# Kernel tuning notes

Measured on AMD Instinct MI355X. Metric: run time of the kernel, lower is better.

The kernel has to match this reference:

```python
import jax, jax.numpy as jnp
import numpy as np

N_NODES = 100000
N_EDGES = 1000000
N_GRAPHS = 128
BN_EPS = 1e-5


def setup_inputs() -> dict:
    key = jax.random.key(0)
    ks = jax.random.split(key, 20)
    H = 64
    F = 128
    C = 10
    inp = {
        'x': jax.random.normal(ks[0], (N_NODES, F), jnp.float32),
        'edge_index': jax.random.randint(ks[1], (2, N_EDGES), 0, N_NODES, jnp.int64),
        'batch': jax.random.randint(ks[2], (N_NODES,), 0, N_GRAPHS, jnp.int64),
        'W1_0': jax.random.normal(ks[3], (F, H), jnp.float32) * 0.05,
        'bn_g_0': jax.random.uniform(ks[4], (H,), jnp.float32) + 0.5,
        'bn_b_0': jax.random.normal(ks[5], (H,), jnp.float32) * 0.1,
        'bn_m_0': jax.random.normal(ks[6], (H,), jnp.float32) * 0.1,
        'bn_v_0': jax.random.uniform(ks[7], (H,), jnp.float32) + 0.5,
        'W2_0': jax.random.normal(ks[8], (H, H), jnp.float32) * 0.1,
        'W1_r': jax.random.normal(ks[9], (3, H, H), jnp.float32) * 0.1,
        'bn_g_r': jax.random.uniform(ks[10], (3, H), jnp.float32) + 0.5,
        'bn_b_r': jax.random.normal(ks[11], (3, H), jnp.float32) * 0.1,
        'bn_m_r': jax.random.normal(ks[12], (3, H), jnp.float32) * 0.1,
        'bn_v_r': jax.random.uniform(ks[13], (3, H), jnp.float32) + 0.5,
        'W2_r': jax.random.normal(ks[14], (3, H, H), jnp.float32) * 0.1,
        'lin1_W': jax.random.normal(ks[15], (H, H), jnp.float32) * 0.1,
        'lin2_W': jax.random.normal(ks[16], (H, C), jnp.float32) * 0.1,
        'lin2_b': jax.random.normal(ks[17], (C,), jnp.float32) * 0.1,
    }
    return inp


def _gin_conv(x, src, dst, W1, g, b, m, v, W2):
    # sum aggregation of neighbor messages (PyG GINConv, eps=0)
    agg = jax.ops.segment_sum(x[src], dst, num_segments=N_NODES)
    h = (x + agg) @ W1                           # [N, H], Linear no bias
    h = (h - m) * jax.lax.rsqrt(v + BN_EPS) * g + b  # BatchNorm1d (eval)
    h = jax.nn.relu(h)
    h = jax.nn.relu(h @ W2)
    return h


def reference(x, edge_index, batch, W1_0, bn_g_0, bn_b_0, bn_m_0, bn_v_0, W2_0,
              W1_r, bn_g_r, bn_b_r, bn_m_r, bn_v_r, W2_r, lin1_W, lin2_W, lin2_b):
    src, dst = edge_index[0], edge_index[1]
    h = _gin_conv(x, src, dst, W1_0, bn_g_0, bn_b_0, bn_m_0, bn_v_0, W2_0)
    for i in range(W1_r.shape[0]):
        h = _gin_conv(h, src, dst, W1_r[i], bn_g_r[i], bn_b_r[i], bn_m_r[i], bn_v_r[i], W2_r[i])
    # global mean pool over graphs
    sums = jax.ops.segment_sum(h, batch, num_segments=N_GRAPHS)
    cnts = jax.ops.segment_sum(jnp.ones((h.shape[0], 1), h.dtype), batch, num_segments=N_GRAPHS)
    pooled = sums / jnp.maximum(cnts, 1.0)
    z = jax.nn.relu(pooled @ lin1_W)  # dropout inactive (eval)
    z = z @ lin2_W + lin2_b
    return jax.nn.log_softmax(z, axis=-1)
```

## Files before the change

### kernel.cpp

```cpp
#include <hip/hip_runtime.h>
#include <hip/hip_bf16.h>
#include <hip/hip_fp16.h>

#define HDIM 64
#define NGRAPH 128
#define NCLS 10
#define BN_EPS 1e-5f
#define SCAN_CHUNK 1024


__global__ void count_kernel(const int* __restrict__ dst, int* __restrict__ deg, int E) {
    int e = blockIdx.x * blockDim.x + threadIdx.x;
    if (e < E) atomicAdd(&deg[dst[e]], 1);
}

__global__ void scan1_kernel(const int* __restrict__ deg, int* __restrict__ part, int N) {
    __shared__ int sh[256];
    int base = blockIdx.x * SCAN_CHUNK + threadIdx.x * 4;
    int s = 0;
#pragma unroll
    for (int i = 0; i < 4; i++) { int idx = base + i; if (idx < N) s += deg[idx]; }
    sh[threadIdx.x] = s; __syncthreads();
    for (int off = 128; off > 0; off >>= 1) {
        if (threadIdx.x < off) sh[threadIdx.x] += sh[threadIdx.x + off];
        __syncthreads();
    }
    if (threadIdx.x == 0) part[blockIdx.x] = sh[0];
}

__global__ void scan2_kernel(int* __restrict__ part, int nblk, int* __restrict__ row_ptr, int N, int E) {
    __shared__ int sh[256];
    int v = (threadIdx.x < nblk) ? part[threadIdx.x] : 0;
    sh[threadIdx.x] = v; __syncthreads();
    for (int off = 1; off < 256; off <<= 1) {
        int t = (threadIdx.x >= off) ? sh[threadIdx.x - off] : 0;
        __syncthreads();
        sh[threadIdx.x] += t;
        __syncthreads();
    }
    if (threadIdx.x < nblk) part[threadIdx.x] = sh[threadIdx.x] - v;
    if (threadIdx.x == 0) row_ptr[N] = E;
}

__global__ void scan3_kernel(const int* __restrict__ deg, const int* __restrict__ part,
                             int* __restrict__ row_ptr, int* __restrict__ cursor, int N) {
    __shared__ int sh[256];
    int tbase = blockIdx.x * SCAN_CHUNK + threadIdx.x * 4;
    int vals[4]; int s = 0;
#pragma unroll
    for (int i = 0; i < 4; i++) { int idx = tbase + i; vals[i] = (idx < N) ? deg[idx] : 0; s += vals[i]; }
    sh[threadIdx.x] = s; __syncthreads();
    for (int off = 1; off < 256; off <<= 1) {
        int t = (threadIdx.x >= off) ? sh[threadIdx.x - off] : 0;
        __syncthreads();
        sh[threadIdx.x] += t;
        __syncthreads();
    }
    int run = part[blockIdx.x] + sh[threadIdx.x] - s;
#pragma unroll
    for (int i = 0; i < 4; i++) {
        int idx = tbase + i;
        if (idx < N) { row_ptr[idx] = run; cursor[idx] = run; run += vals[i]; }
    }
}


__global__ void __launch_bounds__(256) fused_scatter_gemm0_kernel(
        const int* __restrict__ src, const int* __restrict__ dst,
        int* __restrict__ cursor, int* __restrict__ col, int E, int eb,
        const float* __restrict__ X, const float* __restrict__ W,
        __half* __restrict__ Y, int N) {
    __shared__ float Xs[64 * 64];
    __shared__ float Ws[64 * 64];

    if ((int)blockIdx.x < eb) {
        int e = blockIdx.x * 256 + threadIdx.x;
        if (e < E) {
            int pos = atomicAdd(&cursor[dst[e]], 1);
            col[pos] = src[e];
        }
        return;
    }

    const int tid = threadIdx.x;
    const int base = (blockIdx.x - eb) * 64;
    const int ti = tid >> 4;
    const int tj = tid & 15;
    float4 acc[4];
#pragma unroll
    for (int a = 0; a < 4; a++) acc[a] = make_float4(0.f, 0.f, 0.f, 0.f);

    for (int kh = 0; kh < 2; kh++) {
        {
            const float4* Wv = reinterpret_cast<const float4*>(W + kh * 64 * 64);
            float4* Wsv = reinterpret_cast<float4*>(Ws);
            for (int i = tid; i < 1024; i += 256) Wsv[i] = Wv[i];
        }
        for (int i = tid; i < 1024; i += 256) {
            int r = i & 63;
            int c4 = i >> 6;
            int n = base + r;
            float4 v = make_float4(0.f, 0.f, 0.f, 0.f);
            if (n < N) v = *reinterpret_cast<const float4*>(X + (size_t)n * 128 + kh * 64 + c4 * 4);
            Xs[(c4 * 4 + 0) * 64 + r] = v.x;
            Xs[(c4 * 4 + 1) * 64 + r] = v.y;
            Xs[(c4 * 4 + 2) * 64 + r] = v.z;
            Xs[(c4 * 4 + 3) * 64 + r] = v.w;
        }
        __syncthreads();

#pragma unroll 4
        for (int k = 0; k < 64; k++) {
            float4 xv = *reinterpret_cast<const float4*>(&Xs[k * 64 + 4 * ti]);
            float4 wv = *reinterpret_cast<const float4*>(&Ws[k * 64 + 4 * tj]);
            acc[0].x += xv.x * wv.x; acc[0].y += xv.x * wv.y; acc[0].z += xv.x * wv.z; acc[0].w += xv.x * wv.w;
            acc[1].x += xv.y * wv.x; acc[1].y += xv.y * wv.y; acc[1].z += xv.y * wv.z; acc[1].w += xv.y * wv.w;
            acc[2].x += xv.z * wv.x; acc[2].y += xv.z * wv.y; acc[2].z += xv.z * wv.z; acc[2].w += xv.z * wv.w;
            acc[3].x += xv.w * wv.x; acc[3].y += xv.w * wv.y; acc[3].z += xv.w * wv.z; acc[3].w += xv.w * wv.w;
        }
        __syncthreads();
    }

#pragma unroll
    for (int a = 0; a < 4; a++) {
        int n = base + 4 * ti + a;
        if (n < N) {
            __half2* yp = reinterpret_cast<__half2*>(Y + (size_t)n * 64 + 4 * tj);
            yp[0] = __floats2half2_rn(acc[a].x, acc[a].y);
            yp[1] = __floats2half2_rn(acc[a].z, acc[a].w);
        }
    }
}


template<bool RELU>
__global__ void __launch_bounds__(256) gemm_tiled_kernel(const float* __restrict__ X,
                                                         const float* __restrict__ W,
                                                         float* __restrict__ Y, int N) {
    __shared__ float Xs[64 * 64];
    __shared__ float Ws[64 * 64];
    const int tid = threadIdx.x;
    const int base = blockIdx.x * 64;

    {
        const float4* Wv = reinterpret_cast<const float4*>(W);
        float4* Wsv = reinterpret_cast<float4*>(Ws);
        for (int i = tid; i < 1024; i += 256) Wsv[i] = Wv[i];
    }
    for (int i = tid; i < 1024; i += 256) {
        int r = i & 63;
        int c4 = i >> 6;
        int n = base + r;
        float4 v = make_float4(0.f, 0.f, 0.f, 0.f);
        if (n < N) v = *reinterpret_cast<const float4*>(X + (size_t)n * 64 + c4 * 4);
        Xs[(c4 * 4 + 0) * 64 + r] = v.x;
        Xs[(c4 * 4 + 1) * 64 + r] = v.y;
        Xs[(c4 * 4 + 2) * 64 + r] = v.z;
        Xs[(c4 * 4 + 3) * 64 + r] = v.w;
    }
    __syncthreads();

    const int ti = tid >> 4;
    const int tj = tid & 15;
    float4 acc[4];
#pragma unroll
    for (int a = 0; a < 4; a++) acc[a] = make_float4(0.f, 0.f, 0.f, 0.f);

#pragma unroll 4
    for (int k = 0; k < 64; k++) {
        float4 xv = *reinterpret_cast<const float4*>(&Xs[k * 64 + 4 * ti]);
        float4 wv = *reinterpret_cast<const float4*>(&Ws[k * 64 + 4 * tj]);
        acc[0].x += xv.x * wv.x; acc[0].y += xv.x * wv.y; acc[0].z += xv.x * wv.z; acc[0].w += xv.x * wv.w;
        acc[1].x += xv.y * wv.x; acc[1].y += xv.y * wv.y; acc[1].z += xv.y * wv.z; acc[1].w += xv.y * wv.w;
        acc[2].x += xv.z * wv.x; acc[2].y += xv.z * wv.y; acc[2].z += xv.z * wv.z; acc[2].w += xv.z * wv.w;
        acc[3].x += xv.w * wv.x; acc[3].y += xv.w * wv.y; acc[3].z += xv.w * wv.z; acc[3].w += xv.w * wv.w;
    }

#pragma unroll
    for (int a = 0; a < 4; a++) {
        int n = base + 4 * ti + a;
        if (n < N) {
            float4 o = acc[a];
            if (RELU) {
                o.x = fmaxf(o.x, 0.f); o.y = fmaxf(o.y, 0.f);
                o.z = fmaxf(o.z, 0.f); o.w = fmaxf(o.w, 0.f);
            }
            *reinterpret_cast<float4*>(Y + (size_t)n * 64 + 4 * tj) = o;
        }
    }
}


__global__ void __launch_bounds__(256) gemm_pair_kernel(const float* __restrict__ H,
                                                        const float* __restrict__ W2,
                                                        const float* __restrict__ W1n,
                                                        __half* __restrict__ Y, int N) {
    __shared__ float Hs[64 * 64];
    __shared__ float W2s[64 * 64];
    __shared__ float W1s[64 * 64];
    const int tid = threadIdx.x;
    const int base = blockIdx.x * 64;

    {
        const float4* a = reinterpret_cast<const float4*>(W2);
        const float4* c = reinterpret_cast<const float4*>(W1n);
        float4* b = reinterpret_cast<float4*>(W2s);
        float4* d = reinterpret_cast<float4*>(W1s);
        for (int i = tid; i < 1024; i += 256) { b[i] = a[i]; d[i] = c[i]; }
    }
    for (int i = tid; i < 1024; i += 256) {
        int r = i & 63;
        int c4 = i >> 6;
        int n = base + r;
        float4 v = make_float4(0.f, 0.f, 0.f, 0.f);
        if (n < N) v = *reinterpret_cast<const float4*>(H + (size_t)n * 64 + c4 * 4);
        Hs[(c4 * 4 + 0) * 64 + r] = v.x;
        Hs[(c4 * 4 + 1) * 64 + r] = v.y;
        Hs[(c4 * 4 + 2) * 64 + r] = v.z;
        Hs[(c4 * 4 + 3) * 64 + r] = v.w;
    }
    __syncthreads();

    const int ti = tid >> 4;
    const int tj = tid & 15;
    float4 acc[4];
#pragma unroll
    for (int a = 0; a < 4; a++) acc[a] = make_float4(0.f, 0.f, 0.f, 0.f);

#pragma unroll 4
    for (int k = 0; k < 64; k++) {
        float4 xv = *reinterpret_cast<const float4*>(&Hs[k * 64 + 4 * ti]);
        float4 wv = *reinterpret_cast<const float4*>(&W2s[k * 64 + 4 * tj]);
        acc[0].x += xv.x * wv.x; acc[0].y += xv.x * wv.y; acc[0].z += xv.x * wv.z; acc[0].w += xv.x * wv.w;
        acc[1].x += xv.y * wv.x; acc[1].y += xv.y * wv.y; acc[1].z += xv.y * wv.z; acc[1].w += xv.y * wv.w;
        acc[2].x += xv.z * wv.x; acc[2].y += xv.z * wv.y; acc[2].z += xv.z * wv.z; acc[2].w += xv.z * wv.w;
        acc[3].x += xv.w * wv.x; acc[3].y += xv.w * wv.y; acc[3].z += xv.w * wv.z; acc[3].w += xv.w * wv.w;
    }
    __syncthreads();

#pragma unroll
    for (int a = 0; a < 4; a++) {
        float4 o = acc[a];
        o.x = fmaxf(o.x, 0.f); o.y = fmaxf(o.y, 0.f);
        o.z = fmaxf(o.z, 0.f); o.w = fmaxf(o.w, 0.f);
        *reinterpret_cast<float4*>(&Hs[(4 * ti + a) * 64 + 4 * tj]) = o;
    }
    __syncthreads();

    float4 acc2[4];
#pragma unroll
    for (int a = 0; a < 4; a++) acc2[a] = make_float4(0.f, 0.f, 0.f, 0.f);

#pragma unroll 4
    for (int k = 0; k < 64; k++) {
        float z0 = Hs[(4 * ti + 0) * 64 + k];
        float z1 = Hs[(4 * ti + 1) * 64 + k];
        float z2 = Hs[(4 * ti + 2) * 64 + k];
        float z3 = Hs[(4 * ti + 3) * 64 + k];
        float4 wv = *reinterpret_cast<const float4*>(&W1s[k * 64 + 4 * tj]);
        acc2[0].x += z0 * wv.x; acc2[0].y += z0 * wv.y; acc2[0].z += z0 * wv.z; acc2[0].w += z0 * wv.w;
        acc2[1].x += z1 * wv.x; acc2[1].y += z1 * wv.y; acc2[1].z += z1 * wv.z; acc2[1].w += z1 * wv.w;
        acc2[2].x += z2 * wv.x; acc2[2].y += z2 * wv.y; acc2[2].z += z2 * wv.z; acc2[2].w += z2 * wv.w;
        acc2[3].x += z3 * wv.x; acc2[3].y += z3 * wv.y; acc2[3].z += z3 * wv.z; acc2[3].w += z3 * wv.w;
    }

#pragma unroll
    for (int a = 0; a < 4; a++) {
        int n = base + 4 * ti + a;
        if (n < N) {
            __half2* yp = reinterpret_cast<__half2*>(Y + (size_t)n * 64 + 4 * tj);
            yp[0] = __floats2half2_rn(acc2[a].x, acc2[a].y);
            yp[1] = __floats2half2_rn(acc2[a].z, acc2[a].w);
        }
    }
}


__global__ void agg_bn_relu_kernel(const __half* __restrict__ y, const int* __restrict__ rp,
                                   const int* __restrict__ col,
                                   const float* __restrict__ gam, const float* __restrict__ bet,
                                   const float* __restrict__ mu, const float* __restrict__ var,
                                   float* __restrict__ out, int N) {
    int wid = (blockIdx.x * blockDim.x + threadIdx.x) >> 6;
    int lane = threadIdx.x & 63;
    if (wid >= N) return;
    int grp = lane >> 5;
    int fl  = lane & 31;
    int beg = rp[wid], end = rp[wid + 1];

    float2 acc = make_float2(0.f, 0.f);
    if (grp == 0) {
        float2 f = __half22float2(*reinterpret_cast<const __half2*>(y + (size_t)wid * 64 + fl * 2));
        acc.x += f.x; acc.y += f.y;
    }
    int e = beg + grp;
    for (; e + 6 < end; e += 8) {
        int s0 = col[e], s1 = col[e + 2], s2 = col[e + 4], s3 = col[e + 6];
        float2 a0 = __half22float2(*reinterpret_cast<const __half2*>(y + (size_t)s0 * 64 + fl * 2));
        float2 a1 = __half22float2(*reinterpret_cast<const __half2*>(y + (size_t)s1 * 64 + fl * 2));
        float2 a2 = __half22float2(*reinterpret_cast<const __half2*>(y + (size_t)s2 * 64 + fl * 2));
        float2 a3 = __half22float2(*reinterpret_cast<const __half2*>(y + (size_t)s3 * 64 + fl * 2));
        acc.x += a0.x + a1.x + a2.x + a3.x;
        acc.y += a0.y + a1.y + a2.y + a3.y;
    }
    for (; e < end; e += 2) {
        float2 a = __half22float2(*reinterpret_cast<const __half2*>(y + (size_t)col[e] * 64 + fl * 2));
        acc.x += a.x; acc.y += a.y;
    }

    acc.x += __shfl_down(acc.x, 32);
    acc.y += __shfl_down(acc.y, 32);

    if (grp == 0) {
        int f0 = fl * 2, f1 = f0 + 1;
        float sc0 = gam[f0] * rsqrtf(var[f0] + BN_EPS);
        float sc1 = gam[f1] * rsqrtf(var[f1] + BN_EPS);
        float2 o;
        o.x = fmaxf(acc.x * sc0 + (bet[f0] - mu[f0] * sc0), 0.f);
        o.y = fmaxf(acc.y * sc1 + (bet[f1] - mu[f1] * sc1), 0.f);
        *reinterpret_cast<float2*>(out + (size_t)wid * 64 + f0) = o;
    }
}


__global__ void __launch_bounds__(256) pool_partial_kernel(const float* __restrict__ h,
                                                           const int* __restrict__ batch,
                                                           float* __restrict__ partial,
                                                           int* __restrict__ pcnt, int N) {
    __shared__ float ls[NGRAPH * 64];
    __shared__ int lc[NGRAPH];
    for (int i = threadIdx.x; i < NGRAPH * 64; i += 256) ls[i] = 0.f;
    if (threadIdx.x < NGRAPH) lc[threadIdx.x] = 0;
    __syncthreads();
    int lane = threadIdx.x & 63;
    int gwave = blockIdx.x * 4 + (threadIdx.x >> 6);
    int nwaves = gridDim.x * 4;
#pragma unroll 4
    for (int n = gwave; n < N; n += nwaves) {
        int g = batch[n];
        atomicAdd(&ls[g * 64 + lane], h[(size_t)n * 64 + lane]);
        if (lane == 0) atomicAdd(&lc[g], 1);
    }
    __syncthreads();
    for (int i = threadIdx.x; i < NGRAPH * 64; i += 256)
        partial[(size_t)blockIdx.x * NGRAPH * 64 + i] = ls[i];
    if (threadIdx.x < NGRAPH) pcnt[blockIdx.x * NGRAPH + threadIdx.x] = lc[threadIdx.x];
}


__global__ void head_kernel(const float* __restrict__ partial, const int* __restrict__ pcnt, int P,
                            const float* __restrict__ lin1, const float* __restrict__ lin2,
                            const float* __restrict__ b2, float* __restrict__ out) {
    int g = blockIdx.x;
    int j = threadIdx.x;
    __shared__ float p[64];
    __shared__ float z1[64];
    __shared__ float z2[NCLS];
    __shared__ int csh[64];
    float s = 0.f;
    for (int b = 0; b < P; b++) s += partial[(size_t)b * NGRAPH * 64 + g * 64 + j];
    int c = 0;
    for (int b = j; b < P; b += 64) c += pcnt[b * NGRAPH + g];
    csh[j] = c; __syncthreads();
    if (j == 0) { int t = 0; for (int k = 0; k < 64; k++) t += csh[k]; csh[0] = t; }
    __syncthreads();
    float cnt = fmaxf((float)csh[0], 1.f);
    p[j] = s / cnt;
    __syncthreads();
    float a = 0.f;
#pragma unroll
    for (int k = 0; k < 64; k++) a += p[k] * lin1[k * 64 + j];
    z1[j] = fmaxf(a, 0.f);
    __syncthreads();
    if (j < NCLS) {
        float t = b2[j];
#pragma unroll
        for (int k = 0; k < 64; k++) t += z1[k] * lin2[k * NCLS + j];
        z2[j] = t;
    }
    __syncthreads();
    if (j < NCLS) {
        float mx = -1e30f;
#pragma unroll
        for (int c2 = 0; c2 < NCLS; c2++) mx = fmaxf(mx, z2[c2]);
        float se = 0.f;
#pragma unroll
        for (int c2 = 0; c2 < NCLS; c2++) se += expf(z2[c2] - mx);
        out[g * NCLS + j] = z2[j] - mx - logf(se);
    }
}


extern "C" void kernel_launch(void* const* d_in, const int* in_sizes, int n_in,
                              void* d_out, int out_size, void* d_ws, size_t ws_size,
                              hipStream_t stream) {
    const float* x     = (const float*)d_in[0];
    const int*   ei    = (const int*)d_in[1];
    const int*   batch = (const int*)d_in[2];
    const float* W1_0  = (const float*)d_in[3];
    const float* g0    = (const float*)d_in[4];
    const float* b0    = (const float*)d_in[5];
    const float* m0    = (const float*)d_in[6];
    const float* v0    = (const float*)d_in[7];
    const float* W2_0  = (const float*)d_in[8];
    const float* W1r   = (const float*)d_in[9];
    const float* gr    = (const float*)d_in[10];
    const float* br    = (const float*)d_in[11];
    const float* mr    = (const float*)d_in[12];
    const float* vr    = (const float*)d_in[13];
    const float* W2r   = (const float*)d_in[14];
    const float* lin1  = (const float*)d_in[15];
    const float* lin2  = (const float*)d_in[16];
    const float* b2    = (const float*)d_in[17];

    const int N = in_sizes[0] / 128;
    const int E = in_sizes[1] / 2;
    const int* src = ei;
    const int* dst = ei + E;

    char* p = (char*)d_ws;
    auto alloc = [&](size_t bytes) -> char* {
        char* r = p;
        p += (bytes + 255) & ~(size_t)255;
        return r;
    };
    int*    deg     = (int*)alloc((size_t)N * 4);
    int*    row_ptr = (int*)alloc((size_t)(N + 1) * 4);
    int*    cursor  = (int*)alloc((size_t)N * 4);
    int*    col     = (int*)alloc((size_t)E * 4);
    int*    part    = (int*)alloc(256 * 4);
    float*  hA      = (float*)alloc((size_t)N * 64 * 4);
    __half* y16     = (__half*)alloc((size_t)N * 64 * 2);
    size_t used = (size_t)(p - (char*)d_ws);
    size_t per_block = ((size_t)NGRAPH * 64 * 4) + ((size_t)NGRAPH * 4) + 512;
    size_t remain = (ws_size > used) ? (ws_size - used) : 0;
    int P = (int)(remain / per_block);
    if (P > 256) P = 256;
    if (P < 1) P = 1;
    float* partial = (float*)alloc((size_t)P * NGRAPH * 64 * 4);
    int*   pcnt    = (int*)alloc((size_t)P * NGRAPH * 4);
    (void)n_in; (void)out_size;

    hipMemsetAsync(deg, 0, (size_t)N * 4, stream);

    int eb = (E + 255) / 256;
    count_kernel<<<eb, 256, 0, stream>>>(dst, deg, E);
    int nblk = (N + SCAN_CHUNK - 1) / SCAN_CHUNK;
    scan1_kernel<<<nblk, 256, 0, stream>>>(deg, part, N);
    scan2_kernel<<<1, 256, 0, stream>>>(part, nblk, row_ptr, N, E);
    scan3_kernel<<<nblk, 256, 0, stream>>>(deg, part, row_ptr, cursor, N);

    int mb = (N + 63) / 64;
    int ab = (N * 64 + 255) / 256;

    fused_scatter_gemm0_kernel<<<eb + mb, 256, 0, stream>>>(src, dst, cursor, col, E, eb,
                                                            x, W1_0, y16, N);
    agg_bn_relu_kernel<<<ab, 256, 0, stream>>>(y16, row_ptr, col, g0, b0, m0, v0, hA, N);

    gemm_pair_kernel<<<mb, 256, 0, stream>>>(hA, W2_0, W1r, y16, N);
    agg_bn_relu_kernel<<<ab, 256, 0, stream>>>(y16, row_ptr, col, gr, br, mr, vr, hA, N);

    gemm_pair_kernel<<<mb, 256, 0, stream>>>(hA, W2r, W1r + 4096, y16, N);
    agg_bn_relu_kernel<<<ab, 256, 0, stream>>>(y16, row_ptr, col, gr + 64, br + 64, mr + 64, vr + 64, hA, N);

    gemm_pair_kernel<<<mb, 256, 0, stream>>>(hA, W2r + 4096, W1r + 8192, y16, N);
    agg_bn_relu_kernel<<<ab, 256, 0, stream>>>(y16, row_ptr, col, gr + 128, br + 128, mr + 128, vr + 128, hA, N);

    gemm_tiled_kernel<true><<<mb, 256, 0, stream>>>(hA, W2r + 8192, hA, N);

    pool_partial_kernel<<<P, 256, 0, stream>>>(hA, batch, partial, pcnt, N);
    head_kernel<<<NGRAPH, 64, 0, stream>>>(partial, pcnt, P, lin1, lin2, b2, (float*)d_out);
}
```

Measured before the change: 644.7 us.

## Use fp16 MFMA for the 64x64 dense layers with pre-transposed weights

Replaces the FP32 register-tiled SIMT GEMMs (the pair kernel and the last layer) with MFMA 16x16x32 fp16 matrix instructions. A small prep kernel converts and transposes the seven 64x64 weight matrices to fp16 once per call. Activations are cast to fp16 in padded shared memory and accumulated in fp32. The aim is to cut the ALU and LDS cost of the GEMM phases, at the cost of fp16 rounding on inputs and intermediates and one extra launch.

```diff
diff --git a/kernel.cpp b/kernel.cpp
--- a/kernel.cpp
+++ b/kernel.cpp
@@ -7,6 +7,11 @@
 #define NCLS 10
 #define BN_EPS 1e-5f
 #define SCAN_CHUNK 1024
+#define LDH 72
+
+typedef _Float16 h16;
+typedef __attribute__((ext_vector_type(8))) _Float16 f16x8;
+typedef __attribute__((ext_vector_type(4))) float f32x4;
 
 
 __global__ void count_kernel(const int* __restrict__ dst, int* __restrict__ deg, int E) {
@@ -61,6 +66,21 @@
     for (int i = 0; i < 4; i++) {
         int idx = tbase + i;
         if (idx < N) { row_ptr[idx] = run; cursor[idx] = run; run += vals[i]; }
+    }
+}
+
+
+__global__ void prep_weights_kernel(const float* __restrict__ W2_0,
+                                    const float* __restrict__ W2r,
+                                    const float* __restrict__ W1r,
+                                    h16* __restrict__ wt) {
+    int b = blockIdx.x;
+    const float* src = (b == 0) ? W2_0 : (b <= 3) ? W2r + (size_t)(b - 1) * 4096
+                                                  : W1r + (size_t)(b - 4) * 4096;
+    h16* dst = wt + (size_t)b * 4096;
+    for (int i = threadIdx.x; i < 4096; i += 256) {
+        int k = i >> 6, j = i & 63;
+        dst[j * 64 + k] = (h16)src[k * 64 + j];
     }
 }
 
@@ -133,145 +153,148 @@
 }
 
 
-template<bool RELU>
-__global__ void __launch_bounds__(256) gemm_tiled_kernel(const float* __restrict__ X,
-                                                         const float* __restrict__ W,
-                                                         float* __restrict__ Y, int N) {
-    __shared__ float Xs[64 * 64];
-    __shared__ float Ws[64 * 64];
+__global__ void __launch_bounds__(256) gemm_pair_mfma(const float* __restrict__ H,
+                                                      const h16* __restrict__ Wt2,
+                                                      const h16* __restrict__ Wt1,
+                                                      __half* __restrict__ Y, int N) {
+    __shared__ h16 Xs[64 * LDH];
+    __shared__ h16 W2s[64 * LDH];
+    __shared__ h16 W1s[64 * LDH];
     const int tid = threadIdx.x;
     const int base = blockIdx.x * 64;
 
-    {
-        const float4* Wv = reinterpret_cast<const float4*>(W);
-        float4* Wsv = reinterpret_cast<float4*>(Ws);
-        for (int i = tid; i < 1024; i += 256) Wsv[i] = Wv[i];
-    }
-    for (int i = tid; i < 1024; i += 256) {
-        int r = i & 63;
-        int c4 = i >> 6;
-        int n = base + r;
+#pragma unroll
+    for (int it = 0; it < 4; ++it) {
+        int idx = it * 256 + tid;
+        int row = idx >> 4, q = idx & 15;
         float4 v = make_float4(0.f, 0.f, 0.f, 0.f);
-        if (n < N) v = *reinterpret_cast<const float4*>(X + (size_t)n * 64 + c4 * 4);
-        Xs[(c4 * 4 + 0) * 64 + r] = v.x;
-        Xs[(c4 * 4 + 1) * 64 + r] = v.y;
-        Xs[(c4 * 4 + 2) * 64 + r] = v.z;
-        Xs[(c4 * 4 + 3) * 64 + r] = v.w;
-    }
-    __syncthreads();
-
-    const int ti = tid >> 4;
-    const int tj = tid & 15;
-    float4 acc[4];
-#pragma unroll
-    for (int a = 0; a < 4; a++) acc[a] = make_float4(0.f, 0.f, 0.f, 0.f);
-
-#pragma unroll 4
-    for (int k = 0; k < 64; k++) {
-        float4 xv = *reinterpret_cast<const float4*>(&Xs[k * 64 + 4 * ti]);
-        float4 wv = *reinterpret_cast<const float4*>(&Ws[k * 64 + 4 * tj]);
-        acc[0].x += xv.x * wv.x; acc[0].y += xv.x * wv.y; acc[0].z += xv.x * wv.z; acc[0].w += xv.x * wv.w;
-        acc[1].x += xv.y * wv.x; acc[1].y += xv.y * wv.y; acc[1].z += xv.y * wv.z; acc[1].w += xv.y * wv.w;
-        acc[2].x += xv.z * wv.x; acc[2].y += xv.z * wv.y; acc[2].z += xv.z * wv.z; acc[2].w += xv.z * wv.w;
-        acc[3].x += xv.w * wv.x; acc[3].y += xv.w * wv.y; acc[3].z += xv.w * wv.z; acc[3].w += xv.w * wv.w;
-    }
-
-#pragma unroll
-    for (int a = 0; a < 4; a++) {
-        int n = base + 4 * ti + a;
-        if (n < N) {
-            float4 o = acc[a];
-            if (RELU) {
-                o.x = fmaxf(o.x, 0.f); o.y = fmaxf(o.y, 0.f);
-                o.z = fmaxf(o.z, 0.f); o.w = fmaxf(o.w, 0.f);
-            }
-            *reinterpret_cast<float4*>(Y + (size_t)n * 64 + 4 * tj) = o;
-        }
-    }
-}
-
-
-__global__ void __launch_bounds__(256) gemm_pair_kernel(const float* __restrict__ H,
-                                                        const float* __restrict__ W2,
-                                                        const float* __restrict__ W1n,
-                                                        __half* __restrict__ Y, int N) {
-    __shared__ float Hs[64 * 64];
-    __shared__ float W2s[64 * 64];
-    __shared__ float W1s[64 * 64];
+        int n = base + row;
+        if (n < N) v = *reinterpret_cast<const float4*>(H + (size_t)n * 64 + q * 4);
+        h16* d = &Xs[row * LDH + q * 4];
+        d[0] = (h16)v.x; d[1] = (h16)v.y; d[2] = (h16)v.z; d[3] = (h16)v.w;
+    }
+#pragma unroll
+    for (int it = 0; it < 2; ++it) {
+        int idx = it * 256 + tid;
+        int row = idx >> 3, q = idx & 7;
+        *reinterpret_cast<f16x8*>(&W2s[row * LDH + q * 8]) =
+            *reinterpret_cast<const f16x8*>(Wt2 + row * 64 + q * 8);
+        *reinterpret_cast<f16x8*>(&W1s[row * LDH + q * 8]) =
+            *reinterpret_cast<const f16x8*>(Wt1 + row * 64 + q * 8);
+    }
+    __syncthreads();
+
+    const int w  = tid >> 6;
+    const int l  = tid & 63;
+    const int lr = l & 15;
+    const int lk = l >> 4;
+
+    f16x8 a0 = *reinterpret_cast<const f16x8*>(&Xs[(16 * w + lr) * LDH + lk * 8]);
+    f16x8 a1 = *reinterpret_cast<const f16x8*>(&Xs[(16 * w + lr) * LDH + 32 + lk * 8]);
+    f32x4 acc[4];
+#pragma unroll
+    for (int t = 0; t < 4; ++t) {
+        f16x8 b0 = *reinterpret_cast<const f16x8*>(&W2s[(16 * t + lr) * LDH + lk * 8]);
+        f16x8 b1 = *reinterpret_cast<const f16x8*>(&W2s[(16 * t + lr) * LDH + 32 + lk * 8]);
+        f32x4 c = {0.f, 0.f, 0.f, 0.f};
+        c = __builtin_amdgcn_mfma_f32_16x16x32_f16(a0, b0, c, 0, 0, 0);
+        c = __builtin_amdgcn_mfma_f32_16x16x32_f16(a1, b1, c, 0, 0, 0);
+        acc[t] = c;
+    }
+#pragma unroll
+    for (int t = 0; t < 4; ++t)
+#pragma unroll
+        for (int r = 0; r < 4; ++r)
+            Xs[(16 * w + lk * 4 + r) * LDH + 16 * t + lr] = (h16)fmaxf(acc[t][r], 0.f);
+    __syncthreads();
+
+    f16x8 z0 = *reinterpret_cast<const f16x8*>(&Xs[(16 * w + lr) * LDH + lk * 8]);
+    f16x8 z1 = *reinterpret_cast<const f16x8*>(&Xs[(16 * w + lr) * LDH + 32 + lk * 8]);
+    f32x4 acc2[4];
+#pragma unroll
+    for (int t = 0; t < 4; ++t) {
+        f16x8 b0 = *reinterpret_cast<const f16x8*>(&W1s[(16 * t + lr) * LDH + lk * 8]);
+        f16x8 b1 = *reinterpret_cast<const f16x8*>(&W1s[(16 * t + lr) * LDH + 32 + lk * 8]);
+        f32x4 c = {0.f, 0.f, 0.f, 0.f};
+        c = __builtin_amdgcn_mfma_f32_16x16x32_f16(z0, b0, c, 0, 0, 0);
+        c = __builtin_amdgcn_mfma_f32_16x16x32_f16(z1, b1, c, 0, 0, 0);
+        acc2[t] = c;
+    }
+#pragma unroll
+    for (int t = 0; t < 4; ++t)
+#pragma unroll
+        for (int r = 0; r < 4; ++r)
+            W2s[(16 * w + lk * 4 + r) * LDH + 16 * t + lr] = (h16)acc2[t][r];
+    __syncthreads();
+
+#pragma unroll
+    for (int it = 0; it < 2; ++it) {
+        int idx = it * 256 + tid;
+        int row = idx >> 3, q = idx & 7;
+        int n = base + row;
+        if (n < N)
+            *reinterpret_cast<f16x8*>(reinterpret_cast<h16*>(Y) + (size_t)n * 64 + q * 8) =
+                *reinterpret_cast<const f16x8*>(&W2s[row * LDH + q * 8]);
+    }
+}
+
+
+__global__ void __launch_bounds__(256) gemm_last_mfma(const float* __restrict__ H,
+                                                      const h16* __restrict__ Wt,
+                                                      float* __restrict__ Y, int N) {
+    __shared__ h16 Xs[64 * LDH];
+    __shared__ h16 Ws[64 * LDH];
+    __shared__ float Zf[64 * 68];
     const int tid = threadIdx.x;
     const int base = blockIdx.x * 64;
 
-    {
-        const float4* a = reinterpret_cast<const float4*>(W2);
-        const float4* c = reinterpret_cast<const float4*>(W1n);
-        float4* b = reinterpret_cast<float4*>(W2s);
-        float4* d = reinterpret_cast<float4*>(W1s);
-        for (int i = tid; i < 1024; i += 256) { b[i] = a[i]; d[i] = c[i]; }
-    }
-    for (int i = tid; i < 1024; i += 256) {
-        int r = i & 63;
-        int c4 = i >> 6;
-        int n = base + r;
+#pragma unroll
+    for (int it = 0; it < 4; ++it) {
+        int idx = it * 256 + tid;
+        int row = idx >> 4, q = idx & 15;
         float4 v = make_float4(0.f, 0.f, 0.f, 0.f);
-        if (n < N) v = *reinterpret_cast<const float4*>(H + (size_t)n * 64 + c4 * 4);
-        Hs[(c4 * 4 + 0) * 64 + r] = v.x;
-        Hs[(c4 * 4 + 1) * 64 + r] = v.y;
-        Hs[(c4 * 4 + 2) * 64 + r] = v.z;
-        Hs[(c4 * 4 + 3) * 64 + r] = v.w;
-    }
-    __syncthreads();
-
-    const int ti = tid >> 4;
-    const int tj = tid & 15;
-    float4 acc[4];
-#pragma unroll
-    for (int a = 0; a < 4; a++) acc[a] = make_float4(0.f, 0.f, 0.f, 0.f);
-
-#pragma unroll 4
-    for (int k = 0; k < 64; k++) {
-        float4 xv = *reinterpret_cast<const float4*>(&Hs[k * 64 + 4 * ti]);
-        float4 wv = *reinterpret_cast<const float4*>(&W2s[k * 64 + 4 * tj]);
-        acc[0].x += xv.x * wv.x; acc[0].y += xv.x * wv.y; acc[0].z += xv.x * wv.z; acc[0].w += xv.x * wv.w;
-        acc[1].x += xv.y * wv.x; acc[1].y += xv.y * wv.y; acc[1].z += xv.y * wv.z; acc[1].w += xv.y * wv.w;
-        acc[2].x += xv.z * wv.x; acc[2].y += xv.z * wv.y; acc[2].z += xv.z * wv.z; acc[2].w += xv.z * wv.w;
-        acc[3].x += xv.w * wv.x; acc[3].y += xv.w * wv.y; acc[3].z += xv.w * wv.z; acc[3].w += xv.w * wv.w;
-    }
-    __syncthreads();
-
-#pragma unroll
-    for (int a = 0; a < 4; a++) {
-        float4 o = acc[a];
-        o.x = fmaxf(o.x, 0.f); o.y = fmaxf(o.y, 0.f);
-        o.z = fmaxf(o.z, 0.f); o.w = fmaxf(o.w, 0.f);
-        *reinterpret_cast<float4*>(&Hs[(4 * ti + a) * 64 + 4 * tj]) = o;
-    }
-    __syncthreads();
-
-    float4 acc2[4];
-#pragma unroll
-    for (int a = 0; a < 4; a++) acc2[a] = make_float4(0.f, 0.f, 0.f, 0.f);
-
-#pragma unroll 4
-    for (int k = 0; k < 64; k++) {
-        float z0 = Hs[(4 * ti + 0) * 64 + k];
-        float z1 = Hs[(4 * ti + 1) * 64 + k];
-        float z2 = Hs[(4 * ti + 2) * 64 + k];
-        float z3 = Hs[(4 * ti + 3) * 64 + k];
-        float4 wv = *reinterpret_cast<const float4*>(&W1s[k * 64 + 4 * tj]);
-        acc2[0].x += z0 * wv.x; acc2[0].y += z0 * wv.y; acc2[0].z += z0 * wv.z; acc2[0].w += z0 * wv.w;
-        acc2[1].x += z1 * wv.x; acc2[1].y += z1 * wv.y; acc2[1].z += z1 * wv.z; acc2[1].w += z1 * wv.w;
-        acc2[2].x += z2 * wv.x; acc2[2].y += z2 * wv.y; acc2[2].z += z2 * wv.z; acc2[2].w += z2 * wv.w;
-        acc2[3].x += z3 * wv.x; acc2[3].y += z3 * wv.y; acc2[3].z += z3 * wv.z; acc2[3].w += z3 * wv.w;
-    }
-
-#pragma unroll
-    for (int a = 0; a < 4; a++) {
-        int n = base + 4 * ti + a;
-        if (n < N) {
-            __half2* yp = reinterpret_cast<__half2*>(Y + (size_t)n * 64 + 4 * tj);
-            yp[0] = __floats2half2_rn(acc2[a].x, acc2[a].y);
-            yp[1] = __floats2half2_rn(acc2[a].z, acc2[a].w);
-        }
+        int n = base + row;
+        if (n < N) v = *reinterpret_cast<const float4*>(H + (size_t)n * 64 + q * 4);
+        h16* d = &Xs[row * LDH + q * 4];
+        d[0] = (h16)v.x; d[1] = (h16)v.y; d[2] = (h16)v.z; d[3] = (h16)v.w;
+    }
+#pragma unroll
+    for (int it = 0; it < 2; ++it) {
+        int idx = it * 256 + tid;
+        int row = idx >> 3, q = idx & 7;
+        *reinterpret_cast<f16x8*>(&Ws[row * LDH + q * 8]) =
+            *reinterpret_cast<const f16x8*>(Wt + row * 64 + q * 8);
+    }
+    __syncthreads();
+
+    const int w  = tid >> 6;
+    const int l  = tid & 63;
+    const int lr = l & 15;
+    const int lk = l >> 4;
+
+    f16x8 a0 = *reinterpret_cast<const f16x8*>(&Xs[(16 * w + lr) * LDH + lk * 8]);
+    f16x8 a1 = *reinterpret_cast<const f16x8*>(&Xs[(16 * w + lr) * LDH + 32 + lk * 8]);
+#pragma unroll
+    for (int t = 0; t < 4; ++t) {
+        f16x8 b0 = *reinterpret_cast<const f16x8*>(&Ws[(16 * t + lr) * LDH + lk * 8]);
+        f16x8 b1 = *reinterpret_cast<const f16x8*>(&Ws[(16 * t + lr) * LDH + 32 + lk * 8]);
+        f32x4 c = {0.f, 0.f, 0.f, 0.f};
+        c = __builtin_amdgcn_mfma_f32_16x16x32_f16(a0, b0, c, 0, 0, 0);
+        c = __builtin_amdgcn_mfma_f32_16x16x32_f16(a1, b1, c, 0, 0, 0);
+#pragma unroll
+        for (int r = 0; r < 4; ++r)
+            Zf[(16 * w + lk * 4 + r) * 68 + 16 * t + lr] = fmaxf(c[r], 0.f);
+    }
+    __syncthreads();
+
+#pragma unroll
+    for (int it = 0; it < 4; ++it) {
+        int idx = it * 256 + tid;
+        int row = idx >> 4, q = idx & 15;
+        int n = base + row;
+        if (n < N)
+            *reinterpret_cast<float4*>(Y + (size_t)n * 64 + q * 4) =
+                *reinterpret_cast<const float4*>(&Zf[row * 68 + q * 4]);
     }
 }
 
@@ -431,6 +454,7 @@
     int*    part    = (int*)alloc(256 * 4);
     float*  hA      = (float*)alloc((size_t)N * 64 * 4);
     __half* y16     = (__half*)alloc((size_t)N * 64 * 2);
+    h16*    wt      = (h16*)alloc((size_t)7 * 4096 * 2);
     size_t used = (size_t)(p - (char*)d_ws);
     size_t per_block = ((size_t)NGRAPH * 64 * 4) + ((size_t)NGRAPH * 4) + 512;
     size_t remain = (ws_size > used) ? (ws_size - used) : 0;
@@ -443,6 +467,7 @@
 
     hipMemsetAsync(deg, 0, (size_t)N * 4, stream);
 
+    prep_weights_kernel<<<7, 256, 0, stream>>>(W2_0, W2r, W1r, wt);
     int eb = (E + 255) / 256;
     count_kernel<<<eb, 256, 0, stream>>>(dst, deg, E);
     int nblk = (N + SCAN_CHUNK - 1) / SCAN_CHUNK;
@@ -457,16 +482,16 @@
                                                             x, W1_0, y16, N);
     agg_bn_relu_kernel<<<ab, 256, 0, stream>>>(y16, row_ptr, col, g0, b0, m0, v0, hA, N);
 
-    gemm_pair_kernel<<<mb, 256, 0, stream>>>(hA, W2_0, W1r, y16, N);
+    gemm_pair_mfma<<<mb, 256, 0, stream>>>(hA, wt + 0 * 4096, wt + 4 * 4096, y16, N);
     agg_bn_relu_kernel<<<ab, 256, 0, stream>>>(y16, row_ptr, col, gr, br, mr, vr, hA, N);
 
-    gemm_pair_kernel<<<mb, 256, 0, stream>>>(hA, W2r, W1r + 4096, y16, N);
+    gemm_pair_mfma<<<mb, 256, 0, stream>>>(hA, wt + 1 * 4096, wt + 5 * 4096, y16, N);
     agg_bn_relu_kernel<<<ab, 256, 0, stream>>>(y16, row_ptr, col, gr + 64, br + 64, mr + 64, vr + 64, hA, N);
 
-    gemm_pair_kernel<<<mb, 256, 0, stream>>>(hA, W2r + 4096, W1r + 8192, y16, N);
+    gemm_pair_mfma<<<mb, 256, 0, stream>>>(hA, wt + 2 * 4096, wt + 6 * 4096, y16, N);
     agg_bn_relu_kernel<<<ab, 256, 0, stream>>>(y16, row_ptr, col, gr + 128, br + 128, mr + 128, vr + 128, hA, N);
 
-    gemm_tiled_kernel<true><<<mb, 256, 0, stream>>>(hA, W2r + 8192, hA, N);
+    gemm_last_mfma<<<mb, 256, 0, stream>>>(hA, wt + 3 * 4096, hA, N);
 
     pool_partial_kernel<<<P, 256, 0, stream>>>(hA, batch, partial, pcnt, N);
     head_kernel<<<NGRAPH, 64, 0, stream>>>(partial, pcnt, P, lin1, lin2, b2, (float*)d_out);
```

New measurement: 593.2 us. 1.09x faster.
